# Optimization experiments

Hardware: AMD Instinct MI355X
Metric: run time of the kernel (lower is better)

Reference implementation:

```python
import jax, jax.numpy as jnp
import numpy as np
import math

N_HEADS = 16
N_KV_HEADS = 4
D_HEAD = 128
EPS = 1e-6
THETA = 10000.0


def _rmsnorm(x, w):
    var = jnp.mean(x * x, axis=-1, keepdims=True)
    return x * jax.lax.rsqrt(var + EPS) * w


def _rope_tables(S, dtype):
    freqs = 1.0 / THETA ** (jnp.arange(0, D_HEAD, 2, dtype=jnp.float32) / D_HEAD)
    angles = jnp.arange(S, dtype=jnp.float32)[:, None] * freqs[None, :]  # [S, D_HEAD/2]
    angles = jnp.concatenate([angles, angles], axis=-1)  # [S, D_HEAD]
    return jnp.cos(angles).astype(dtype), jnp.sin(angles).astype(dtype)


def _apply_rope(x, cos, sin):
    # x: [B, H, S, D]; rotate-half convention matching cat([angles, angles])
    half = D_HEAD // 2
    x1, x2 = x[..., :half], x[..., half:]
    rot = jnp.concatenate([-x2, x1], axis=-1)
    return x * cos[None, None] + rot * sin[None, None]


def setup_inputs() -> dict:
    key = jax.random.key(0)
    ks = jax.random.split(key, 5)
    B, S, D = 2, 2048, 2048
    s = 0.02
    return {
        "x": jax.random.normal(ks[0], (B, S, D), jnp.float32),
        "Wq": jax.random.normal(ks[1], (D, N_HEADS * D_HEAD), jnp.float32) * s,
        "Wk": jax.random.normal(ks[2], (D, N_KV_HEADS * D_HEAD), jnp.float32) * s,
        "Wv": jax.random.normal(ks[3], (D, N_KV_HEADS * D_HEAD), jnp.float32) * s,
        "Wo": jax.random.normal(ks[4], (D, D), jnp.float32) * s,
        "q_norm_w": jnp.ones((D_HEAD,), jnp.float32),
        "k_norm_w": jnp.ones((D_HEAD,), jnp.float32),
    }


def reference(x, Wq, Wk, Wv, Wo, q_norm_w, k_norm_w):
    B, S, D = x.shape
    groups = N_HEADS // N_KV_HEADS

    q = (x @ Wq).reshape(B, S, N_HEADS, D_HEAD).transpose(0, 2, 1, 3)      # [B,H,S,d]
    k = (x @ Wk).reshape(B, S, N_KV_HEADS, D_HEAD).transpose(0, 2, 1, 3)   # [B,Hkv,S,d]
    v = (x @ Wv).reshape(B, S, N_KV_HEADS, D_HEAD).transpose(0, 2, 1, 3)

    q = _rmsnorm(q, q_norm_w)
    k = _rmsnorm(k, k_norm_w)

    cos, sin = _rope_tables(S, x.dtype)
    q = _apply_rope(q, cos, sin)
    k = _apply_rope(k, cos, sin)

    # GQA broadcast: repeat kv heads into query head dim
    k = jnp.repeat(k, groups, axis=1)  # [B,H,S,d]
    v = jnp.repeat(v, groups, axis=1)

    scale = 1.0 / math.sqrt(D_HEAD)
    scores = jnp.einsum("bhqd,bhkd->bhqk", q, k) * scale
    causal = jnp.tril(jnp.ones((S, S), bool))
    scores = jnp.where(causal[None, None], scores, jnp.finfo(scores.dtype).min)
    probs = jax.nn.softmax(scores, axis=-1)
    out = jnp.einsum("bhqk,bhkd->bhqd", probs, v)  # [B,H,S,d]
    out = out.transpose(0, 2, 1, 3).reshape(B, S, D)
    return out @ Wo
```

## Files before the change

### kernel.cpp

```cpp
#include <hip/hip_runtime.h>
#include <stdint.h>

typedef __attribute__((ext_vector_type(8))) short bf16x8;
typedef __attribute__((ext_vector_type(4))) float f32x4;
typedef __attribute__((ext_vector_type(16))) float f32x16;
typedef unsigned short u16;
typedef unsigned int   u32;
typedef unsigned long long u64;

#define S_LEN 2048
#define NH    16
#define NKV   4
#define DH    128
#define DM    2048
#define QKV_N 3072
#define MROWS 4096

__device__ __forceinline__ u16 f2bf(float x) {
  u32 u = __float_as_uint(x);
  return (u16)((u + 0x7fffu + ((u >> 16) & 1u)) >> 16);
}
__device__ __forceinline__ float bf2f(u16 h) {
  return __uint_as_float(((u32)h) << 16);
}
__device__ __forceinline__ u32 cvtpk(float lo, float hi) {
  u32 r;
  asm("v_cvt_pk_bf16_f32 %0, %1, %2" : "=v"(r) : "v"(lo), "v"(hi));
  return r;
}
__device__ __forceinline__ void plswap(u32& a, u32& b) {
  asm volatile("v_permlane32_swap_b32 %0, %1" : "+v"(a), "+v"(b));
}
__device__ __forceinline__ void gload_lds16(const void* g, void* l) {
  __builtin_amdgcn_global_load_lds((const __attribute__((address_space(1))) void*)g,
                                   (__attribute__((address_space(3))) void*)l, 16, 0, 0);
}

__global__ void __launch_bounds__(256) convert_x_kernel(const float* __restrict__ x,
                                                        u16* __restrict__ o) {
  int idx = (blockIdx.x * 256 + threadIdx.x) * 8;
  float4 a = *(const float4*)(x + idx);
  float4 b = *(const float4*)(x + idx + 4);
  union { u16 s[8]; uint4 v; } t;
  t.s[0] = f2bf(a.x); t.s[1] = f2bf(a.y); t.s[2] = f2bf(a.z); t.s[3] = f2bf(a.w);
  t.s[4] = f2bf(b.x); t.s[5] = f2bf(b.y); t.s[6] = f2bf(b.z); t.s[7] = f2bf(b.w);
  *(uint4*)(o + idx) = t.v;
}

__global__ void __launch_bounds__(256) transpose_w_kernel(const float* __restrict__ src,
                                                          u16* __restrict__ dst, int N) {
  __shared__ float t[64][65];
  const int bx = blockIdx.x, by = blockIdx.y, tid = threadIdx.x;
#pragma unroll
  for (int rep = 0; rep < 16; ++rep) {
    int lin = rep * 256 + tid;
    int i = lin >> 6, jj = lin & 63;
    t[i][jj] = src[(size_t)(bx * 64 + i) * N + by * 64 + jj];
  }
  __syncthreads();
#pragma unroll
  for (int rep = 0; rep < 16; ++rep) {
    int lin = rep * 256 + tid;
    int nr = lin >> 6, kc = lin & 63;
    dst[(size_t)(by * 64 + nr) * DM + bx * 64 + kc] = f2bf(t[kc][nr]);
  }
}

__global__ void __launch_bounds__(256) rope_tables_kernel(float* __restrict__ ct,
                                                          float* __restrict__ st_) {
  int idx = blockIdx.x * 256 + threadIdx.x;
  int s = idx >> 6, i = idx & 63;
  const float L2_10000 = 13.287712379549449f;
  float freq = exp2f(-(float)i * (1.0f / 64.0f) * L2_10000);
  float ang = (float)s * freq;
  ct[idx] = cosf(ang);
  st_[idx] = sinf(ang);
}

template <int OUTF32>
__global__ void __launch_bounds__(256) gemm_bt(const u16* __restrict__ A,
                                               const u16* __restrict__ Bt,
                                               void* __restrict__ C,
                                               int M, int N, int K) {
  __shared__ __align__(16) u16 As[128 * 32];
  __shared__ __align__(16) u16 Bs[128 * 32];
  const int tid = threadIdx.x;
  const int w = tid >> 6, l = tid & 63;
  const int g = l >> 4, q15 = l & 15;
  const int row0 = blockIdx.y * 128, col0 = blockIdx.x * 128;
  const int wm = (w >> 1) * 64, wn = (w & 1) * 64;
  const f32x4 fz = {0.f, 0.f, 0.f, 0.f};
  f32x4 acc[4][4];
#pragma unroll
  for (int m = 0; m < 4; ++m)
#pragma unroll
    for (int n = 0; n < 4; ++n) acc[m][n] = fz;

  for (int kt = 0; kt < K; kt += 32) {
#pragma unroll
    for (int c = 0; c < 2; ++c) {
      int P = (w * 2 + c) * 1024;
      int Pl = P + l * 16;
      int arow = Pl >> 6, acolb = Pl & 63;
      gload_lds16((const char*)A + ((size_t)(row0 + arow) * K + kt) * 2 + acolb,
                  (char*)As + P);
      gload_lds16((const char*)Bt + ((size_t)(col0 + arow) * K + kt) * 2 + acolb,
                  (char*)Bs + P);
    }
    __syncthreads();
    bf16x8 af[4], bfv[4];
#pragma unroll
    for (int m = 0; m < 4; ++m)
      af[m] = *(const bf16x8*)((const char*)As + (wm + m * 16 + q15) * 64 + g * 16);
#pragma unroll
    for (int n = 0; n < 4; ++n)
      bfv[n] = *(const bf16x8*)((const char*)Bs + (wn + n * 16 + q15) * 64 + g * 16);
#pragma unroll
    for (int m = 0; m < 4; ++m)
#pragma unroll
      for (int n = 0; n < 4; ++n)
        acc[m][n] = __builtin_amdgcn_mfma_f32_16x16x32_bf16(af[m], bfv[n], acc[m][n], 0, 0, 0);
    __syncthreads();
  }
#pragma unroll
  for (int m = 0; m < 4; ++m)
#pragma unroll
    for (int n = 0; n < 4; ++n)
#pragma unroll
      for (int r = 0; r < 4; ++r) {
        int rr = row0 + wm + m * 16 + g * 4 + r;
        int cc = col0 + wn + n * 16 + q15;
        float v = acc[m][n][r];
        if (OUTF32) ((float*)C)[(size_t)rr * N + cc] = v;
        else        ((u16*)C)[(size_t)rr * N + cc]  = f2bf(v);
      }
}

__global__ void __launch_bounds__(256) norm_rope_kernel(const u16* __restrict__ qkv,
                                                        const float* __restrict__ qw,
                                                        const float* __restrict__ kw,
                                                        const float* __restrict__ ct,
                                                        const float* __restrict__ st_,
                                                        u16* __restrict__ Qo,
                                                        u16* __restrict__ Ko) {
  int wid = blockIdx.x * 4 + (threadIdx.x >> 6);
  int l = threadIdx.x & 63;
  int row = wid / 20;
  int j = wid - row * 20;
  int b = row >> 11, s = row & 2047;
  bool isq = j < 16;
  int h = isq ? j : (j - 16);
  const u16* src = qkv + (size_t)row * QKV_N + (isq ? h * DH : (2048 + h * DH));
  float x1 = bf2f(src[l]), x2 = bf2f(src[l + 64]);
  float ss = x1 * x1 + x2 * x2;
#pragma unroll
  for (int off = 32; off > 0; off >>= 1) ss += __shfl_xor(ss, off);
  float rn = rsqrtf(ss * (1.0f / 128.0f) + 1e-6f);
  const float* wv = isq ? qw : kw;
  float n1 = x1 * rn * wv[l], n2 = x2 * rn * wv[l + 64];
  float cv = ct[s * 64 + l], sv = st_[s * 64 + l];
  float o1 = n1 * cv - n2 * sv;
  float o2 = n2 * cv + n1 * sv;
  float scale = isq ? 0.08838834764831845f : 1.0f;
  u16* dst = isq ? (Qo + ((size_t)(b * NH + h) * S_LEN + s) * DH)
                 : (Ko + ((size_t)(b * NKV + h) * S_LEN + s) * DH);
  dst[l]      = f2bf(o1 * scale);
  dst[l + 64] = f2bf(o2 * scale);
}

__global__ void __launch_bounds__(256) vtrans_kernel(const u16* __restrict__ qkv,
                                                     u16* __restrict__ vt) {
  __shared__ u16 t[64][65];
  const int st = blockIdx.x, dt = blockIdx.y, bz = blockIdx.z;
  const int tid = threadIdx.x;
#pragma unroll
  for (int rep = 0; rep < 16; ++rep) {
    int lin = rep * 256 + tid;
    int i = lin >> 6, jj = lin & 63;
    t[i][jj] = qkv[(size_t)((bz >> 2) * S_LEN + st * 64 + i) * QKV_N
                   + 2560 + (bz & 3) * DH + dt * 64 + jj];
  }
  __syncthreads();
#pragma unroll
  for (int rep = 0; rep < 16; ++rep) {
    int lin = rep * 256 + tid;
    int dr = lin >> 6, sc = lin & 63;
    vt[((size_t)bz * DH + dt * 64 + dr) * S_LEN + st * 64 + sc] = t[sc][dr];
  }
}

__global__ void __launch_bounds__(256, 2) attn_kernel(const u16* __restrict__ Qg,
                                                      const u16* __restrict__ Kg,
                                                      const u16* __restrict__ Vt,
                                                      u16* __restrict__ O) {
  __shared__ __align__(16) char smem[65536];
  const int tid = threadIdx.x;
  const int w = tid >> 6, l = tid & 63;
  const int q31 = l & 31, hi = l >> 5;
  const int id = blockIdx.x;
  const int grp = id & 7;
  const int mem = (id >> 3) & 3;
  const int pr  = id >> 5;
  const int b   = grp >> 2, kvh = grp & 3;
  const int h   = kvh * 4 + mem;

  const char* Kbase = (const char*)(Kg + (size_t)(b * NKV + kvh) * S_LEN * DH);
  const char* Vbase = (const char*)(Vt + (size_t)(b * NKV + kvh) * DH * S_LEN);

  auto stage = [&](int buf, int kt) {
    char* Ksb = smem + buf * 32768;
    char* Vsb = Ksb + 16384;
    const char* Kt  = Kbase + (size_t)kt * 64 * 256;
    const char* Vtb = Vbase + (size_t)kt * 128;
#pragma unroll
    for (int i = 0; i < 4; ++i) {
      int off = w * 4096 + i * 1024 + l * 16;
      int row = off >> 8;
      {
        int cb = (off & 255) ^ ((row & 15) << 4);
        gload_lds16(Kt + (size_t)row * 256 + cb, Ksb + off); }
      {
        int qoff = (off & 255) ^ ((row & 15) << 4);
        int d = row * 2 + (qoff >> 7);
        int kvb = qoff & 127;
        gload_lds16(Vtb + (size_t)d * (S_LEN * 2) + kvb, Vsb + off); }
    }
  };

  stage(0, 0);
  int cur = 0;

  for (int pass = 0; pass < 2; ++pass) {
    const int tq  = pass ? (15 - pr) : pr;
    const int qb  = tq * 128;
    const int nkt = 2 * tq + 1;
    const int qg  = qb + w * 32 + q31;

    bf16x8 qreg[8];
    const u16* Qrow = Qg + ((size_t)(b * NH + h) * S_LEN + qg) * DH;
#pragma unroll
    for (int c = 0; c < 8; ++c)
      qreg[c] = *(const bf16x8*)(Qrow + c * 16 + hi * 8);

    f32x16 acc[4];
#pragma unroll
    for (int dt = 0; dt < 4; ++dt)
#pragma unroll
      for (int r = 0; r < 16; ++r) acc[dt][r] = 0.f;
    float mrun = -1e30f, lrun = 0.f;

    for (int kt = 0; kt <= nkt; ++kt) {
      if (kt < nkt) {
        stage(cur ^ 1, kt + 1);
        asm volatile("s_waitcnt vmcnt(8)" ::: "memory");
      } else if (pass == 0) {
        stage(cur ^ 1, 0);
        asm volatile("s_waitcnt vmcnt(8)" ::: "memory");
      } else {
        asm volatile("s_waitcnt vmcnt(0)" ::: "memory");
      }
      __builtin_amdgcn_sched_barrier(0);
      __builtin_amdgcn_s_barrier();

      const char* Ks = smem + cur * 32768;
      const char* Vs = Ks + 16384;

      f32x16 sa[2];
#pragma unroll
      for (int s = 0; s < 2; ++s)
#pragma unroll
        for (int r = 0; r < 16; ++r) sa[s][r] = 0.f;
      __builtin_amdgcn_s_setprio(1);
#pragma unroll
      for (int s = 0; s < 2; ++s) {
        int krow = s * 32 + q31;
        const char* kr = Ks + krow * 256;
        int sw = (krow & 15) << 4;
#pragma unroll
        for (int c = 0; c < 8; ++c) {
          bf16x8 kf = *(const bf16x8*)(kr + ((c * 32 + hi * 16) ^ sw));
          sa[s] = __builtin_amdgcn_mfma_f32_32x32x16_bf16(kf, qreg[c], sa[s], 0, 0, 0);
        }
      }
      __builtin_amdgcn_s_setprio(0);

      const bool domask = (kt * 64 + 63) > (qb + w * 32);
      float tmax = -1e30f;
#pragma unroll
      for (int s = 0; s < 2; ++s)
#pragma unroll
        for (int r = 0; r < 16; ++r) {
          float v = sa[s][r];
          if (domask) {
            int kvg = kt * 64 + s * 32 + (r & 3) + 8 * (r >> 2) + 4 * hi;
            if (kvg > qg) v = -1e30f;
          }
          sa[s][r] = v;
          tmax = fmaxf(tmax, v);
        }
      tmax = fmaxf(tmax, __shfl_xor(tmax, 32));

      const bool defer = __all(tmax <= mrun + 8.0f);
      const float mnew = defer ? mrun : fmaxf(mrun, tmax);

      float tsum = 0.f;
      union { u32 u[4]; bf16x8 v; } pf[4];
#pragma unroll
      for (int s = 0; s < 2; ++s)
#pragma unroll
        for (int kl = 0; kl < 2; ++kl) {
          float e0 = __expf(sa[s][kl * 8 + 0] - mnew);
          float e1 = __expf(sa[s][kl * 8 + 1] - mnew);
          float e2 = __expf(sa[s][kl * 8 + 2] - mnew);
          float e3 = __expf(sa[s][kl * 8 + 3] - mnew);
          float e4 = __expf(sa[s][kl * 8 + 4] - mnew);
          float e5 = __expf(sa[s][kl * 8 + 5] - mnew);
          float e6 = __expf(sa[s][kl * 8 + 6] - mnew);
          float e7 = __expf(sa[s][kl * 8 + 7] - mnew);
          tsum += (e0 + e1) + (e2 + e3) + (e4 + e5) + (e6 + e7);
          u32 A0 = cvtpk(e0, e1), A1 = cvtpk(e2, e3);
          u32 B0 = cvtpk(e4, e5), B1 = cvtpk(e6, e7);
          plswap(A0, B0);
          plswap(A1, B1);
          int ks = s * 2 + kl;
          pf[ks].u[0] = A0; pf[ks].u[1] = A1; pf[ks].u[2] = B0; pf[ks].u[3] = B1;
        }
      tsum += __shfl_xor(tsum, 32);

      if (defer) {
        lrun += tsum;
      } else {
        float alpha = __expf(mrun - mnew);
        lrun = lrun * alpha + tsum;
        mrun = mnew;
#pragma unroll
        for (int dt = 0; dt < 4; ++dt)
#pragma unroll
          for (int r = 0; r < 16; ++r) acc[dt][r] *= alpha;
      }

      __builtin_amdgcn_s_setprio(1);
#pragma unroll
      for (int dt = 0; dt < 4; ++dt) {
        int d = dt * 32 + q31;
        int vrow = d >> 1;
        const char* vr = Vs + vrow * 256;
        int sw = (vrow & 15) << 4;
        int hb = (d & 1) << 7;
#pragma unroll
        for (int ks = 0; ks < 4; ++ks) {
          bf16x8 vf = *(const bf16x8*)(vr + ((hb | (ks * 32 + hi * 16)) ^ sw));
          acc[dt] = __builtin_amdgcn_mfma_f32_32x32x16_bf16(vf, pf[ks].v, acc[dt], 0, 0, 0);
        }
      }
      __builtin_amdgcn_s_setprio(0);

      __builtin_amdgcn_s_barrier();
      cur ^= 1;
    }

    const float linv = 1.0f / lrun;
    u16* Obase = O + ((size_t)b * S_LEN + qg) * DM + h * DH;
#pragma unroll
    for (int dt = 0; dt < 4; ++dt)
#pragma unroll
      for (int rg = 0; rg < 4; ++rg) {
        int d0 = dt * 32 + rg * 8 + hi * 4;
        u32 w0 = cvtpk(acc[dt][rg * 4 + 0] * linv, acc[dt][rg * 4 + 1] * linv);
        u32 w1 = cvtpk(acc[dt][rg * 4 + 2] * linv, acc[dt][rg * 4 + 3] * linv);
        u64 vv = (u64)w0 | ((u64)w1 << 32);
        *(u64*)(Obase + d0) = vv;
      }
  }
}

extern "C" void kernel_launch(void* const* d_in, const int* in_sizes, int n_in,
                              void* d_out, int out_size, void* d_ws, size_t ws_size,
                              hipStream_t stream) {
  (void)in_sizes; (void)n_in; (void)out_size; (void)ws_size;
  const float* x  = (const float*)d_in[0];
  const float* Wq = (const float*)d_in[1];
  const float* Wk = (const float*)d_in[2];
  const float* Wv = (const float*)d_in[3];
  const float* Wo = (const float*)d_in[4];
  const float* qw = (const float*)d_in[5];
  const float* kw = (const float*)d_in[6];

  char* ws = (char*)d_ws;
  u16*   xb    = (u16*)(ws + 0);
  u16*   wqkvt = (u16*)(ws + 16777216);
  u16*   wot   = (u16*)(ws + 29360128);
  u16*   qo    = (u16*)(ws + 37748736);
  u16*   ko    = (u16*)(ws + 54525952);
  u16*   vt    = (u16*)(ws + 58720256);
  float* ctab  = (float*)(ws + 62914560);
  float* stab  = (float*)(ws + 63438848);
  u16*   qkvp  = (u16*)d_out;
  u16*   attn  = (u16*)(ws + 0);
  float* outp  = (float*)d_out;

  convert_x_kernel<<<4096, 256, 0, stream>>>(x, xb);
  transpose_w_kernel<<<dim3(32, 32), 256, 0, stream>>>(Wq, wqkvt, 2048);
  transpose_w_kernel<<<dim3(32, 8),  256, 0, stream>>>(Wk, wqkvt + (size_t)2048 * 2048, 512);
  transpose_w_kernel<<<dim3(32, 8),  256, 0, stream>>>(Wv, wqkvt + (size_t)2560 * 2048, 512);
  transpose_w_kernel<<<dim3(32, 32), 256, 0, stream>>>(Wo, wot, 2048);
  rope_tables_kernel<<<512, 256, 0, stream>>>(ctab, stab);

  gemm_bt<0><<<dim3(24, 32), 256, 0, stream>>>(xb, wqkvt, qkvp, MROWS, QKV_N, DM);
  norm_rope_kernel<<<20480, 256, 0, stream>>>(qkvp, qw, kw, ctab, stab, qo, ko);
  vtrans_kernel<<<dim3(32, 2, 8), 256, 0, stream>>>(qkvp, vt);
  attn_kernel<<<256, 256, 0, stream>>>(qo, ko, vt, attn);
  gemm_bt<1><<<dim3(16, 32), 256, 0, stream>>>(attn, wot, outp, MROWS, DM, DM);
}
```

Baseline: 244.0 us.

## Split attention KV range across two blocks with atomic-flag merge

Doubles the attention grid so that each query tile's KV range is split between two blocks. Each block writes unnormalized bf16 partial outputs plus running max and sum to scratch, and the second block to finish (detected via an atomic counter) merges the two partials with log-sum-exp weights. The aim is to fill more CUs on the MI355X than 256 blocks can. In exchange it adds extra global traffic, a memset, fences, and some precision loss from storing partials in bf16.

After: 470.6 us. 1.93x slower.

```diff
diff --git a/kernel.cpp b/kernel.cpp
--- a/kernel.cpp
+++ b/kernel.cpp
@@ -192,15 +192,20 @@
 __global__ void __launch_bounds__(256, 2) attn_kernel(const u16* __restrict__ Qg,
                                                       const u16* __restrict__ Kg,
                                                       const u16* __restrict__ Vt,
-                                                      u16* __restrict__ O) {
+                                                      u16* __restrict__ partO,
+                                                      float* __restrict__ mlbuf,
+                                                      u32* __restrict__ flags,
+                                                      u16* __restrict__ Oout) {
   __shared__ __align__(16) char smem[65536];
+  __shared__ u32 who;
   const int tid = threadIdx.x;
   const int w = tid >> 6, l = tid & 63;
   const int q31 = l & 31, hi = l >> 5;
   const int id = blockIdx.x;
   const int grp = id & 7;
   const int mem = (id >> 3) & 3;
-  const int pr  = id >> 5;
+  const int pr  = (id >> 5) & 7;
+  const int hf  = id >> 8;
   const int b   = grp >> 2, kvh = grp & 3;
   const int h   = kvh * 4 + mem;
 
@@ -227,14 +232,16 @@
     }
   };
 
-  stage(0, 0);
+  stage(0, hf ? (pr + 1) : 0);
   int cur = 0;
 
   for (int pass = 0; pass < 2; ++pass) {
-    const int tq  = pass ? (15 - pr) : pr;
-    const int qb  = tq * 128;
-    const int nkt = 2 * tq + 1;
-    const int qg  = qb + w * 32 + q31;
+    const int tq   = pass ? (15 - pr) : pr;
+    const int kbeg = pass ? (hf ? (16 - pr) : 0) : (hf ? (pr + 1) : 0);
+    const int kend = pass ? (hf ? (31 - 2 * pr) : (15 - pr)) : (hf ? (2 * pr + 1) : pr);
+    const int loB  = hf ? (16 - pr) : 0;
+    const int qb   = tq * 128;
+    const int qg   = qb + w * 32 + q31;
 
     bf16x8 qreg[8];
     const u16* Qrow = Qg + ((size_t)(b * NH + h) * S_LEN + qg) * DH;
@@ -249,12 +256,12 @@
       for (int r = 0; r < 16; ++r) acc[dt][r] = 0.f;
     float mrun = -1e30f, lrun = 0.f;
 
-    for (int kt = 0; kt <= nkt; ++kt) {
-      if (kt < nkt) {
+    for (int kt = kbeg; kt <= kend; ++kt) {
+      if (kt < kend) {
         stage(cur ^ 1, kt + 1);
         asm volatile("s_waitcnt vmcnt(8)" ::: "memory");
       } else if (pass == 0) {
-        stage(cur ^ 1, 0);
+        stage(cur ^ 1, loB);
         asm volatile("s_waitcnt vmcnt(8)" ::: "memory");
       } else {
         asm volatile("s_waitcnt vmcnt(0)" ::: "memory");
@@ -293,7 +300,7 @@
           float v = sa[s][r];
           if (domask) {
             int kvg = kt * 64 + s * 32 + (r & 3) + 8 * (r >> 2) + 4 * hi;
-            if (kvg > qg) v = -1e30f;
+            if (kvg > qg) v = -3.0e38f;
           }
           sa[s][r] = v;
           tmax = fmaxf(tmax, v);
@@ -359,18 +366,52 @@
       cur ^= 1;
     }
 
-    const float linv = 1.0f / lrun;
-    u16* Obase = O + ((size_t)b * S_LEN + qg) * DM + h * DH;
+    size_t prow = (size_t)(b * NH + h) * S_LEN + qg;
+    u16* Pb = partO + ((size_t)hf * 65536 + prow) * 128;
 #pragma unroll
     for (int dt = 0; dt < 4; ++dt)
 #pragma unroll
       for (int rg = 0; rg < 4; ++rg) {
         int d0 = dt * 32 + rg * 8 + hi * 4;
-        u32 w0 = cvtpk(acc[dt][rg * 4 + 0] * linv, acc[dt][rg * 4 + 1] * linv);
-        u32 w1 = cvtpk(acc[dt][rg * 4 + 2] * linv, acc[dt][rg * 4 + 3] * linv);
-        u64 vv = (u64)w0 | ((u64)w1 << 32);
-        *(u64*)(Obase + d0) = vv;
-      }
+        u32 w0 = cvtpk(acc[dt][rg * 4 + 0], acc[dt][rg * 4 + 1]);
+        u32 w1 = cvtpk(acc[dt][rg * 4 + 2], acc[dt][rg * 4 + 3]);
+        *(u64*)(Pb + d0) = (u64)w0 | ((u64)w1 << 32);
+      }
+    if (hi == 0) {
+      float2 ml; ml.x = mrun; ml.y = lrun;
+      *(float2*)(mlbuf + ((size_t)hf * 65536 + prow) * 2) = ml;
+    }
+    __threadfence();
+    __syncthreads();
+    if (tid == 0) who = atomicAdd(&flags[(b * NH + h) * 16 + tq], 1u);
+    __syncthreads();
+
+    if (who == 1) {
+      __threadfence();
+      int r  = tid >> 1;
+      int cg = (tid & 1) * 64;
+      size_t rowi = (size_t)(b * NH + h) * S_LEN + qb + r;
+      const u16* P0 = partO + rowi * 128;
+      const u16* P1 = partO + ((size_t)65536 + rowi) * 128;
+      float2 ml0 = *(const float2*)(mlbuf + rowi * 2);
+      float2 ml1 = *(const float2*)(mlbuf + ((size_t)65536 + rowi) * 2);
+      float ms = fmaxf(ml0.x, ml1.x);
+      float w0 = __expf(ml0.x - ms), w1 = __expf(ml1.x - ms);
+      float dn = 1.0f / (ml0.y * w0 + ml1.y * w1);
+      u16* Ob = Oout + ((size_t)b * S_LEN + qb + r) * DM + h * DH + cg;
+#pragma unroll
+      for (int j = 0; j < 64; j += 4) {
+        u64 a0 = *(const u64*)(P0 + cg + j);
+        u64 a1 = *(const u64*)(P1 + cg + j);
+        float f0 = bf2f((u16)(a0 >> 0))  * w0 + bf2f((u16)(a1 >> 0))  * w1;
+        float f1 = bf2f((u16)(a0 >> 16)) * w0 + bf2f((u16)(a1 >> 16)) * w1;
+        float f2 = bf2f((u16)(a0 >> 32)) * w0 + bf2f((u16)(a1 >> 32)) * w1;
+        float f3 = bf2f((u16)(a0 >> 48)) * w0 + bf2f((u16)(a1 >> 48)) * w1;
+        u32 o0 = cvtpk(f0 * dn, f1 * dn);
+        u32 o1 = cvtpk(f2 * dn, f3 * dn);
+        *(u64*)(Ob + j) = (u64)o0 | ((u64)o1 << 32);
+      }
+    }
   }
 }
 
@@ -395,9 +436,14 @@
   u16*   vt    = (u16*)(ws + 58720256);
   float* ctab  = (float*)(ws + 62914560);
   float* stab  = (float*)(ws + 63438848);
+  u32*   flags = (u32*)(ws + 63963136);
   u16*   qkvp  = (u16*)d_out;
   u16*   attn  = (u16*)(ws + 0);
+  u16*   partO = (u16*)d_out;
+  float* mlbuf = (float*)(ws + 16777216);
   float* outp  = (float*)d_out;
+
+  hipMemsetAsync(flags, 0, 2048, stream);
 
   convert_x_kernel<<<4096, 256, 0, stream>>>(x, xb);
   transpose_w_kernel<<<dim3(32, 32), 256, 0, stream>>>(Wq, wqkvt, 2048);
@@ -409,6 +455,6 @@
   gemm_bt<0><<<dim3(24, 32), 256, 0, stream>>>(xb, wqkvt, qkvp, MROWS, QKV_N, DM);
   norm_rope_kernel<<<20480, 256, 0, stream>>>(qkvp, qw, kw, ctab, stab, qo, ko);
   vtrans_kernel<<<dim3(32, 2, 8), 256, 0, stream>>>(qkvp, vt);
-  attn_kernel<<<256, 256, 0, stream>>>(qo, ko, vt, attn);
+  attn_kernel<<<512, 256, 0, stream>>>(qo, ko, vt, partO, mlbuf, flags, attn);
   gemm_bt<1><<<dim3(16, 32), 256, 0, stream>>>(attn, wot, outp, MROWS, DM, DM);
 }
```
